# Optimization experiments

Hardware: AMD Instinct MI355X
Metric: run time of the kernel (lower is better)

The kernel has to match this reference:

```python
import jax, jax.numpy as jnp
import numpy as np
from jax import lax

B, C, IMG, P = 32, 3, 224, 16
W, L, H, E = 768, 12, 12, 512
S = (IMG // P) ** 2 + 1  # 197
HD = W // H  # 64
FF = 4 * W


def _make_pe():
    pos = np.arange(S, dtype=np.float64)[:, None]
    i = np.arange(W, dtype=np.float64)[None, :]
    angle = pos / 10000.0 ** ((i - (i % 2)) / W)
    pe = np.where(i % 2 == 0, np.sin(angle), np.cos(angle))
    return jnp.asarray(pe[None], dtype=jnp.float32)  # [1,S,W]


def setup_inputs() -> dict:
    key = jax.random.key(0)
    ks = iter(jax.random.split(key, 32))
    g = lambda shape, s=0.02: jax.random.normal(next(ks), shape, jnp.float32) * s
    return {
        "x": jax.random.normal(next(ks), (B, C, IMG, IMG), jnp.float32),
        "conv_w": g((W, C, P, P)),
        "conv_b": jnp.zeros((W,), jnp.float32),
        "cls_token": g((1, 1, W), 1.0),
        "pe": _make_pe(),
        "ln1_g": jnp.ones((L, W), jnp.float32),
        "ln1_b": jnp.zeros((L, W), jnp.float32),
        "wq": g((L, W, W)), "bq": jnp.zeros((L, W), jnp.float32),
        "wk": g((L, W, W)), "bk": jnp.zeros((L, W), jnp.float32),
        "wv": g((L, W, W)), "bv": jnp.zeros((L, W), jnp.float32),
        "wo": g((L, W, W)), "bo": jnp.zeros((L, W), jnp.float32),
        "ln2_g": jnp.ones((L, W), jnp.float32),
        "ln2_b": jnp.zeros((L, W), jnp.float32),
        "w1": g((L, W, FF)), "b1": jnp.zeros((L, FF), jnp.float32),
        "w2": g((L, FF, W)), "b2": jnp.zeros((L, W), jnp.float32),
        "proj": g((W, E), 1.0),
    }


def _layernorm(x, gamma, beta, eps=1e-5):
    m = jnp.mean(x, axis=-1, keepdims=True)
    v = jnp.mean((x - m) ** 2, axis=-1, keepdims=True)
    return (x - m) * lax.rsqrt(v + eps) * gamma + beta


def _forward(x, conv_w, conv_b, cls_token, pe, ln1_g, ln1_b, wq, bq, wk, bk,
             wv, bv, wo, bo, ln2_g, ln2_b, w1, b1, w2, b2, proj):
    # patch embedding: conv stride = patch size
    p = lax.conv_general_dilated(x, conv_w, (P, P), 'VALID',
                                 dimension_numbers=('NCHW', 'OIHW', 'NCHW'))
    p = p + conv_b[None, :, None, None]
    tokens = p.reshape(p.shape[0], W, -1).transpose(0, 2, 1)  # [B, n_patches, W]
    cls = jnp.broadcast_to(cls_token, (tokens.shape[0], 1, W))
    h = jnp.concatenate([cls, tokens], axis=1) + pe  # [B,S,W]

    def block(h, params):
        (g1, b1_, Wq, Bq, Wk, Bk, Wv, Bv, Wo, Bo, g2, b2_, W1, B1, W2, B2) = params
        y = _layernorm(h, g1, b1_)
        q = (y @ Wq + Bq).reshape(-1, S, H, HD)
        k = (y @ Wk + Bk).reshape(-1, S, H, HD)
        v = (y @ Wv + Bv).reshape(-1, S, H, HD)
        att = jnp.einsum('bshd,bthd->bhst', q, k) / jnp.sqrt(jnp.float32(HD))
        att = jax.nn.softmax(att, axis=-1)
        o = jnp.einsum('bhst,bthd->bshd', att, v).reshape(-1, S, W)
        h = h + o @ Wo + Bo
        y = _layernorm(h, g2, b2_)
        h = h + jax.nn.gelu(y @ W1 + B1, approximate=False) @ W2 + B2
        return h, None

    stacked = (ln1_g, ln1_b, wq, bq, wk, bk, wv, bv, wo, bo,
               ln2_g, ln2_b, w1, b1, w2, b2)
    h, _ = lax.scan(block, h, stacked)
    out = h[:, 0] @ proj  # [B,E]
    return out / jnp.linalg.norm(out, axis=-1, keepdims=True)


def reference(x, conv_w, conv_b, cls_token, pe, ln1_g, ln1_b, wq, bq, wk, bk,
              wv, bv, wo, bo, ln2_g, ln2_b, w1, b1, w2, b2, proj):
    return _forward(x, conv_w, conv_b, cls_token, pe, ln1_g, ln1_b, wq, bq,
                    wk, bk, wv, bv, wo, bo, ln2_g, ln2_b, w1, b1, w2, b2, proj)
```

## Files before the change

### kernel.cpp

```cpp
#include <hip/hip_runtime.h>
#include <math.h>

#define NB 32
#define SEQ 197
#define WD 768
#define NH 12
#define HD 64
#define FF 3072
#define NL 12
#define ROWS (NB*SEQ)
#define MPAD 6400
#define PROWS (NB*196)

typedef __attribute__((ext_vector_type(8))) short short8x;
typedef __attribute__((ext_vector_type(4))) float f32x4;

__device__ __forceinline__ ushort f2bf(float f) {
  unsigned u = __builtin_bit_cast(unsigned, f);
  u += 0x7fffu + ((u >> 16) & 1u);
  return (ushort)(u >> 16);
}

__device__ __forceinline__ void gload16(const ushort* g, ushort* l) {
  __builtin_amdgcn_global_load_lds(
      (const __attribute__((address_space(1))) void*)g,
      (__attribute__((address_space(3))) void*)l, 16, 0, 0);
}

__device__ __forceinline__ float wave_sum(float v) {
  #pragma unroll
  for (int off = 32; off; off >>= 1) v += __shfl_xor(v, off);
  return v;
}

template<int EPI>
__global__ __launch_bounds__(256) void gemm_bt(
    const ushort* __restrict__ A, const ushort* __restrict__ Bt,
    const float* __restrict__ bias, const float* __restrict__ R,
    float* __restrict__ Cf, ushort* __restrict__ Cb,
    int M, int N, int K)
{
  __shared__ __align__(16) ushort As[128*32];
  __shared__ __align__(16) ushort Bs[128*32];
  const int tid = threadIdx.x;
  const int gx = gridDim.x;
  const int nwg = gx * gridDim.y;
  const int orig = blockIdx.y * gx + blockIdx.x;
  const int xcd = orig & 7, lin = orig >> 3;
  const int qq = nwg >> 3, rr = nwg & 7;
  const int id = xcd*qq + (xcd < rr ? xcd : rr) + lin;
  const int bm = (id / gx) * 128;
  const int bn = (id % gx) * 128;

  const int w = tid >> 6, ln = tid & 63;
  const int wr = (w >> 1) * 64, wc = (w & 1) * 64;
  const int srow = tid >> 2, skoff = (tid & 3) * 8;
  const ushort* Ap = A + (size_t)(bm + srow) * K + skoff;
  const ushort* Bp = Bt + (size_t)(bn + srow) * K + skoff;
  ushort* AsW = As + w * 512;
  ushort* BsW = Bs + w * 512;
  const size_t half = (size_t)64 * K;
  const int fr = ln & 15, kg = ln >> 4;

  f32x4 acc[4][4];
  #pragma unroll
  for (int m = 0; m < 4; ++m)
    #pragma unroll
    for (int n = 0; n < 4; ++n) acc[m][n] = (f32x4){0.f, 0.f, 0.f, 0.f};

  for (int k0 = 0; k0 < K; k0 += 32) {
    __syncthreads();
    gload16(Ap + k0, AsW);
    gload16(Ap + half + k0, AsW + 2048);
    gload16(Bp + k0, BsW);
    gload16(Bp + half + k0, BsW + 2048);
    __syncthreads();
    short8x av[4], bv[4];
    #pragma unroll
    for (int m = 0; m < 4; ++m)
      av[m] = *(const short8x*)&As[(wr + m*16 + fr)*32 + kg*8];
    #pragma unroll
    for (int n = 0; n < 4; ++n)
      bv[n] = *(const short8x*)&Bs[(wc + n*16 + fr)*32 + kg*8];
    #pragma unroll
    for (int m = 0; m < 4; ++m)
      #pragma unroll
      for (int n = 0; n < 4; ++n)
        acc[m][n] = __builtin_amdgcn_mfma_f32_16x16x32_bf16(av[m], bv[n], acc[m][n], 0, 0, 0);
  }

  const int crow = bm + wr + kg*4;
  const int ccol = bn + wc + fr;
  float bi[4];
  #pragma unroll
  for (int n = 0; n < 4; ++n) bi[n] = bias[ccol + n*16];
  #pragma unroll
  for (int m = 0; m < 4; ++m) {
    #pragma unroll
    for (int j = 0; j < 4; ++j) {
      const int r = crow + m*16 + j;
      if (r < M) {
        #pragma unroll
        for (int n = 0; n < 4; ++n) {
          const size_t off = (size_t)r * N + ccol + n*16;
          float vv = acc[m][n][j] + bi[n];
          if (EPI == 0) Cf[off] = vv;
          if (EPI == 1) Cf[off] = vv + R[off];
          if (EPI == 2) Cb[off] = f2bf(0.5f * vv * (1.f + erff(vv * 0.70710678118654752f)));
          if (EPI == 3) Cb[off] = f2bf(vv);
        }
      }
    }
  }
}

__global__ __launch_bounds__(256) void attn_fused(
    const ushort* __restrict__ qkv,
    ushort* __restrict__ obf)
{
  __shared__ __align__(16) ushort KP[208*72];
  __shared__ __align__(16) ushort Vt[64*232];
  const int tid = threadIdx.x;
  const int w = tid >> 6, l = tid & 63;
  const int fr = l & 15, kg = l >> 4;
  const int orig = blockIdx.y * 4 + blockIdx.x;
  const int id = (orig & 7) * 192 + (orig >> 3);
  const int qt = id & 3;
  const int bh = id >> 2;
  const int b = bh / 12, hh = bh - b*12;
  const size_t qrow0 = (size_t)b * SEQ;
  const ushort* kbase = qkv + qrow0*2304 + 768 + hh*64;
  const ushort* vbase = qkv + qrow0*2304 + 1536 + hh*64;

  #pragma unroll
  for (int it = 0; it < 7; ++it) {
    const int idx = it*256 + tid;
    if (idx < 1664) {
      const int row = idx >> 3, kc = (idx & 7) << 3;
      short8x v = (short8x){0,0,0,0,0,0,0,0};
      if (row < SEQ) v = *(const short8x*)(kbase + (size_t)row*2304 + kc);
      *(short8x*)&KP[row*72 + kc] = v;
    }
  }
  #pragma unroll
  for (int it = 0; it < 7; ++it) {
    const int t = it*32 + (tid & 31);
    const int dc = ((tid >> 5) & 7) << 3;
    short8x v = (short8x){0,0,0,0,0,0,0,0};
    if (t < SEQ) v = *(const short8x*)(vbase + (size_t)t*2304 + dc);
    #pragma unroll
    for (int j = 0; j < 8; ++j) Vt[(dc + j)*232 + t] = (ushort)v[j];
  }
  const int s_l = qt*64 + w*16 + fr;
  const ushort* qbase = qkv + (qrow0 + (s_l < SEQ ? s_l : SEQ-1))*2304 + hh*64;
  const short8x qf0 = *(const short8x*)(qbase + kg*8);
  const short8x qf1 = *(const short8x*)(qbase + 32 + kg*8);
  __syncthreads();

  f32x4 sacc[13];
  #pragma unroll
  for (int f = 0; f < 13; ++f) sacc[f] = (f32x4){0.f,0.f,0.f,0.f};
  #pragma unroll
  for (int f = 0; f < 13; ++f) {
    const short8x kf0 = *(const short8x*)&KP[(f*16 + fr)*72 + kg*8];
    const short8x kf1 = *(const short8x*)&KP[(f*16 + fr)*72 + 32 + kg*8];
    sacc[f] = __builtin_amdgcn_mfma_f32_16x16x32_bf16(qf0, kf0, sacc[f], 0, 0, 0);
    sacc[f] = __builtin_amdgcn_mfma_f32_16x16x32_bf16(qf1, kf1, sacc[f], 0, 0, 0);
  }
  float mx[4] = {-1e30f,-1e30f,-1e30f,-1e30f};
  #pragma unroll
  for (int f = 0; f < 13; ++f)
    #pragma unroll
    for (int j = 0; j < 4; ++j) {
      float v = sacc[f][j] * 0.125f;
      if (f == 12 && fr >= 5) v = -1e30f;
      sacc[f][j] = v;
      mx[j] = fmaxf(mx[j], v);
    }
  #pragma unroll
  for (int j = 0; j < 4; ++j) {
    mx[j] = fmaxf(mx[j], __shfl_xor(mx[j], 1));
    mx[j] = fmaxf(mx[j], __shfl_xor(mx[j], 2));
    mx[j] = fmaxf(mx[j], __shfl_xor(mx[j], 4));
    mx[j] = fmaxf(mx[j], __shfl_xor(mx[j], 8));
  }
  float sm[4] = {0.f,0.f,0.f,0.f};
  #pragma unroll
  for (int f = 0; f < 13; ++f)
    #pragma unroll
    for (int j = 0; j < 4; ++j) {
      const float e = __expf(sacc[f][j] - mx[j]);
      sacc[f][j] = e; sm[j] += e;
    }
  #pragma unroll
  for (int j = 0; j < 4; ++j) {
    sm[j] += __shfl_xor(sm[j], 1);
    sm[j] += __shfl_xor(sm[j], 2);
    sm[j] += __shfl_xor(sm[j], 4);
    sm[j] += __shfl_xor(sm[j], 8);
    sm[j] = 1.f / sm[j];
  }
  __syncthreads();
  ushort* P = &KP[w*16*232];
  #pragma unroll
  for (int f = 0; f < 13; ++f)
    #pragma unroll
    for (int j = 0; j < 4; ++j)
      P[(kg*4 + j)*232 + f*16 + fr] = f2bf(sacc[f][j] * sm[j]);
  #pragma unroll
  for (int j = 0; j < 4; ++j)
    P[(kg*4 + j)*232 + 208 + fr] = 0;
  __syncthreads();

  short8x pf[7];
  #pragma unroll
  for (int tc = 0; tc < 7; ++tc)
    pf[tc] = *(const short8x*)&P[fr*232 + tc*32 + kg*8];
  f32x4 oacc[4];
  #pragma unroll
  for (int df = 0; df < 4; ++df) oacc[df] = (f32x4){0.f,0.f,0.f,0.f};
  #pragma unroll
  for (int df = 0; df < 4; ++df)
    #pragma unroll
    for (int tc = 0; tc < 7; ++tc) {
      const short8x vf = *(const short8x*)&Vt[(df*16 + fr)*232 + tc*32 + kg*8];
      oacc[df] = __builtin_amdgcn_mfma_f32_16x16x32_bf16(pf[tc], vf, oacc[df], 0, 0, 0);
    }
  #pragma unroll
  for (int df = 0; df < 4; ++df)
    #pragma unroll
    for (int j = 0; j < 4; ++j) {
      const int s = qt*64 + w*16 + kg*4 + j;
      if (s < SEQ)
        obf[(qrow0 + s)*768 + hh*64 + df*16 + fr] = f2bf(oacc[df][j]);
    }
}

__global__ void tcast_k(const float* __restrict__ in, ushort* __restrict__ out,
                        int K, int N) {
  __shared__ float t[32][33];
  const int bx = blockIdx.x * 32, by = blockIdx.y * 32;
  const int tx = threadIdx.x, ty = threadIdx.y;
  #pragma unroll
  for (int j = 0; j < 32; j += 8)
    t[ty + j][tx] = in[(size_t)(by + ty + j) * N + bx + tx];
  __syncthreads();
  #pragma unroll
  for (int j = 0; j < 32; j += 8)
    out[(size_t)(bx + ty + j) * K + by + tx] = f2bf(t[tx][ty + j]);
}

__global__ void tcast4_k(const float* __restrict__ s0, const float* __restrict__ s1,
                         const float* __restrict__ s2, const float* __restrict__ s3,
                         ushort* __restrict__ d0, ushort* __restrict__ d1,
                         ushort* __restrict__ d2, ushort* __restrict__ d3) {
  const int z = blockIdx.z;
  const float* s = (z == 0) ? s0 : (z == 1) ? s1 : (z == 2) ? s2 : s3;
  ushort* d = (z == 0) ? d0 : (z == 1) ? d1 : (z == 2) ? d2 : d3;
  __shared__ float t[32][33];
  const int bx = blockIdx.x * 32, by = blockIdx.y * 32;
  const int tx = threadIdx.x, ty = threadIdx.y;
  #pragma unroll
  for (int j = 0; j < 32; j += 8)
    t[ty + j][tx] = s[(size_t)(by + ty + j) * WD + bx + tx];
  __syncthreads();
  #pragma unroll
  for (int j = 0; j < 32; j += 8)
    d[(size_t)(bx + ty + j) * WD + by + tx] = f2bf(t[tx][ty + j]);
}

__global__ void castcv_k(const float* __restrict__ in, ushort* __restrict__ out) {
  const int i = blockIdx.x * 256 + threadIdx.x;
  out[i] = f2bf(in[i]);
}

__global__ void bcat_k(const float* __restrict__ a, const float* __restrict__ b,
                       const float* __restrict__ c, float* __restrict__ d) {
  const int i = blockIdx.x * 256 + threadIdx.x;
  if (i < 2304) d[i] = (i < 768) ? a[i] : (i < 1536) ? b[i - 768] : c[i - 1536];
}

__global__ void im2col_k(const float* __restrict__ x, ushort* __restrict__ A) {
  const int idx = blockIdx.x * 256 + threadIdx.x;
  if (idx >= PROWS * WD) return;
  const int k = idx % WD;
  const int row = idx / WD;
  const int pw = k & 15, ph = (k >> 4) & 15, c = k >> 8;
  const int px = row % 14, py = (row / 14) % 14, b = row / 196;
  A[idx] = f2bf(x[(size_t)((b*3 + c)*224 + py*16 + ph) * 224 + px*16 + pw]);
}

__global__ void assemble_k(const float* __restrict__ tok, const float* __restrict__ cls,
                           const float* __restrict__ pe, float* __restrict__ h) {
  const int idx = blockIdx.x * 256 + threadIdx.x;
  if (idx >= ROWS * WD) return;
  const int w = idx % WD;
  const int bs = idx / WD;
  const int s = bs % SEQ;
  const int b = bs / SEQ;
  float v;
  if (s == 0) v = cls[w];
  else        v = tok[(size_t)(b*196 + s - 1) * WD + w];
  h[idx] = v + pe[(size_t)s * WD + w];
}

__global__ __launch_bounds__(256) void layernorm_k(
    const float* __restrict__ x, const float* __restrict__ g,
    const float* __restrict__ bb, ushort* __restrict__ y)
{
  const int row = blockIdx.x;
  const int tid = threadIdx.x;
  const float* xr = x + (size_t)row * WD;
  const float v0 = xr[tid], v1 = xr[tid+256], v2 = xr[tid+512];
  __shared__ float red[4];
  float s = v0 + v1 + v2;
  s = wave_sum(s);
  const int wv = tid >> 6, ln = tid & 63;
  if (ln == 0) red[wv] = s;
  __syncthreads();
  const float mean = (red[0]+red[1]+red[2]+red[3]) * (1.f/768.f);
  const float d0 = v0-mean, d1 = v1-mean, d2 = v2-mean;
  float sq = d0*d0 + d1*d1 + d2*d2;
  sq = wave_sum(sq);
  __syncthreads();
  if (ln == 0) red[wv] = sq;
  __syncthreads();
  const float var = (red[0]+red[1]+red[2]+red[3]) * (1.f/768.f);
  const float inv = rsqrtf(var + 1e-5f);
  ushort* yr = y + (size_t)row * WD;
  yr[tid]     = f2bf(d0 * inv * g[tid]     + bb[tid]);
  yr[tid+256] = f2bf(d1 * inv * g[tid+256] + bb[tid+256]);
  yr[tid+512] = f2bf(d2 * inv * g[tid+512] + bb[tid+512]);
}

__global__ __launch_bounds__(256) void head_k(
    const float* __restrict__ h, const float* __restrict__ proj,
    float* __restrict__ out)
{
  const int b = blockIdx.x;
  const int tid = threadIdx.x;
  __shared__ float hr[768];
  __shared__ float red[4];
  const float* hrow = h + (size_t)b * SEQ * WD;
  hr[tid] = hrow[tid]; hr[tid+256] = hrow[tid+256]; hr[tid+512] = hrow[tid+512];
  __syncthreads();
  float o0 = 0.f, o1 = 0.f;
  for (int kx = 0; kx < 768; ++kx) {
    const float hv = hr[kx];
    o0 = fmaf(hv, proj[(size_t)kx*512 + tid],       o0);
    o1 = fmaf(hv, proj[(size_t)kx*512 + tid + 256], o1);
  }
  float sq = o0*o0 + o1*o1;
  sq = wave_sum(sq);
  const int wv = tid >> 6, ln = tid & 63;
  if (ln == 0) red[wv] = sq;
  __syncthreads();
  const float inv = 1.f / sqrtf(red[0]+red[1]+red[2]+red[3]);
  out[(size_t)b*512 + tid]       = o0 * inv;
  out[(size_t)b*512 + tid + 256] = o1 * inv;
}

extern "C" void kernel_launch(void* const* d_in, const int* in_sizes, int n_in,
                              void* d_out, int out_size, void* d_ws, size_t ws_size,
                              hipStream_t stream) {
  const float* x      = (const float*)d_in[0];
  const float* conv_w = (const float*)d_in[1];
  const float* conv_b = (const float*)d_in[2];
  const float* cls    = (const float*)d_in[3];
  const float* pe     = (const float*)d_in[4];
  const float* ln1_g  = (const float*)d_in[5];
  const float* ln1_b  = (const float*)d_in[6];
  const float* wq = (const float*)d_in[7];  const float* bq = (const float*)d_in[8];
  const float* wk = (const float*)d_in[9];  const float* bk = (const float*)d_in[10];
  const float* wvw = (const float*)d_in[11]; const float* bv = (const float*)d_in[12];
  const float* wo = (const float*)d_in[13]; const float* bo = (const float*)d_in[14];
  const float* ln2_g = (const float*)d_in[15]; const float* ln2_b = (const float*)d_in[16];
  const float* w1 = (const float*)d_in[17]; const float* b1 = (const float*)d_in[18];
  const float* w2 = (const float*)d_in[19]; const float* b2 = (const float*)d_in[20];
  const float* proj = (const float*)d_in[21];
  float* out = (float*)d_out;

  float* ws = (float*)d_ws;
  const size_t TOK = (size_t)ROWS * WD;
  float* h = ws;
  ushort* ub = (ushort*)(ws + TOK);
  ushort* ybf    = ub;  ub += (size_t)MPAD * WD;
  ushort* qkv    = ub;  ub += (size_t)MPAD * 2304;
  ushort* obf    = ub;  ub += (size_t)MPAD * WD;
  ushort* zbf    = ub;  ub += (size_t)MPAD * FF;
  ushort* wt_qkv = ub;  ub += (size_t)2304 * WD;
  ushort* wt_o   = ub;  ub += (size_t)WD * WD;
  ushort* wt_1   = ub;  ub += (size_t)WD * FF;
  ushort* wt_2   = ub;  ub += (size_t)FF * WD;
  float* bqkv = (float*)ub;  ub += 4608;
  ushort* imbf   = zbf;
  float*  ypatch = (float*)(zbf + (size_t)PROWS * WD);
  ushort* cbf    = wt_qkv;

  castcv_k<<<dim3(2304), dim3(256), 0, stream>>>(conv_w, cbf);
  im2col_k<<<dim3((PROWS*WD)/256), dim3(256), 0, stream>>>(x, imbf);
  gemm_bt<0><<<dim3(6, 49), dim3(256), 0, stream>>>(
      imbf, cbf, conv_b, nullptr, ypatch, nullptr, PROWS, WD, WD);
  assemble_k<<<dim3((ROWS*WD)/256), dim3(256), 0, stream>>>(ypatch, cls, pe, h);

  const dim3 gqkv(18, 50);
  const dim3 g768(6, 50);
  const dim3 gff(24, 50);
  const dim3 gattn(4, NB*NH);
  const dim3 tdim(32, 8);

  for (int l = 0; l < NL; ++l) {
    const size_t wOff = (size_t)l * WD * WD;
    const size_t fOff = (size_t)l * WD * FF;
    const size_t vOff = (size_t)l * WD;
    const size_t fvOff = (size_t)l * FF;

    tcast4_k<<<dim3(24,24,4), tdim, 0, stream>>>(
        wq+wOff, wk+wOff, wvw+wOff, wo+wOff,
        wt_qkv, wt_qkv + 589824, wt_qkv + 1179648, wt_o);
    tcast_k<<<dim3(96,24), tdim, 0, stream>>>(w1+fOff, wt_1, WD, FF);
    tcast_k<<<dim3(24,96), tdim, 0, stream>>>(w2+fOff, wt_2, FF, WD);
    bcat_k<<<dim3(9), dim3(256), 0, stream>>>(bq+vOff, bk+vOff, bv+vOff, bqkv);

    layernorm_k<<<dim3(ROWS), dim3(256), 0, stream>>>(h, ln1_g+vOff, ln1_b+vOff, ybf);
    gemm_bt<3><<<gqkv, dim3(256), 0, stream>>>(ybf, wt_qkv, bqkv, nullptr,
                                               nullptr, qkv, ROWS, 2304, WD);
    attn_fused<<<gattn, dim3(256), 0, stream>>>(qkv, obf);
    gemm_bt<1><<<g768, dim3(256), 0, stream>>>(obf, wt_o, bo+vOff, h, h, nullptr, ROWS, WD, WD);
    layernorm_k<<<dim3(ROWS), dim3(256), 0, stream>>>(h, ln2_g+vOff, ln2_b+vOff, ybf);
    gemm_bt<2><<<gff, dim3(256), 0, stream>>>(ybf, wt_1, b1+fvOff, nullptr,
                                              nullptr, zbf, ROWS, FF, WD);
    gemm_bt<1><<<g768, dim3(256), 0, stream>>>(zbf, wt_2, b2+vOff, h, h, nullptr, ROWS, WD, FF);
  }

  head_k<<<dim3(NB), dim3(256), 0, stream>>>(h, proj, out);
}
```

Before: 3.540 ms.

## Double-buffer GEMM LDS tiles and split-K the N=768 projections with combine kernel

The GEMM mainloop now double-buffers its LDS tiles, issuing the next K-slice's global-to-LDS loads before computing the current one, so there is one barrier per iteration instead of two. The two N=768 GEMMs (attention output projection and FFN down-projection) are split over K into two halves via blockIdx.z. This doubles their grid from 300 workgroups, which is meant to fill the MI355X CUs better. The halves write fp32 partial planes, and a new combine kernel adds both partials, the bias and the residual into h. The split adds extra global traffic for the partials and extra launches, and doubles LDS use per block, which may lower occupancy.

```diff
diff --git a/kernel.cpp b/kernel.cpp
--- a/kernel.cpp
+++ b/kernel.cpp
@@ -38,10 +38,10 @@
     const ushort* __restrict__ A, const ushort* __restrict__ Bt,
     const float* __restrict__ bias, const float* __restrict__ R,
     float* __restrict__ Cf, ushort* __restrict__ Cb,
-    int M, int N, int K)
+    int M, int N, int K, int kspl)
 {
-  __shared__ __align__(16) ushort As[128*32];
-  __shared__ __align__(16) ushort Bs[128*32];
+  __shared__ __align__(16) ushort As[2][128*32];
+  __shared__ __align__(16) ushort Bs[2][128*32];
   const int tid = threadIdx.x;
   const int gx = gridDim.x;
   const int nwg = gx * gridDim.y;
@@ -51,14 +51,14 @@
   const int id = xcd*qq + (xcd < rr ? xcd : rr) + lin;
   const int bm = (id / gx) * 128;
   const int bn = (id % gx) * 128;
+  const int koff = blockIdx.z * kspl;
 
   const int w = tid >> 6, ln = tid & 63;
   const int wr = (w >> 1) * 64, wc = (w & 1) * 64;
   const int srow = tid >> 2, skoff = (tid & 3) * 8;
-  const ushort* Ap = A + (size_t)(bm + srow) * K + skoff;
-  const ushort* Bp = Bt + (size_t)(bn + srow) * K + skoff;
-  ushort* AsW = As + w * 512;
-  ushort* BsW = Bs + w * 512;
+  const ushort* Ap = A + (size_t)(bm + srow) * K + skoff + koff;
+  const ushort* Bp = Bt + (size_t)(bn + srow) * K + skoff + koff;
+  const int lofs = w * 512;
   const size_t half = (size_t)64 * K;
   const int fr = ln & 15, kg = ln >> 4;
 
@@ -68,32 +68,43 @@
     #pragma unroll
     for (int n = 0; n < 4; ++n) acc[m][n] = (f32x4){0.f, 0.f, 0.f, 0.f};
 
-  for (int k0 = 0; k0 < K; k0 += 32) {
-    __syncthreads();
-    gload16(Ap + k0, AsW);
-    gload16(Ap + half + k0, AsW + 2048);
-    gload16(Bp + k0, BsW);
-    gload16(Bp + half + k0, BsW + 2048);
-    __syncthreads();
+  gload16(Ap,        &As[0][lofs]);
+  gload16(Ap + half, &As[0][lofs + 2048]);
+  gload16(Bp,        &Bs[0][lofs]);
+  gload16(Bp + half, &Bs[0][lofs + 2048]);
+  __syncthreads();
+
+  const int nt = kspl >> 5;
+  for (int t = 0; t < nt; ++t) {
+    const int cur = t & 1;
+    if (t + 1 < nt) {
+      const int k1 = (t + 1) << 5;
+      gload16(Ap + k1,        &As[cur ^ 1][lofs]);
+      gload16(Ap + half + k1, &As[cur ^ 1][lofs + 2048]);
+      gload16(Bp + k1,        &Bs[cur ^ 1][lofs]);
+      gload16(Bp + half + k1, &Bs[cur ^ 1][lofs + 2048]);
+    }
     short8x av[4], bv[4];
     #pragma unroll
     for (int m = 0; m < 4; ++m)
-      av[m] = *(const short8x*)&As[(wr + m*16 + fr)*32 + kg*8];
+      av[m] = *(const short8x*)&As[cur][(wr + m*16 + fr)*32 + kg*8];
     #pragma unroll
     for (int n = 0; n < 4; ++n)
-      bv[n] = *(const short8x*)&Bs[(wc + n*16 + fr)*32 + kg*8];
+      bv[n] = *(const short8x*)&Bs[cur][(wc + n*16 + fr)*32 + kg*8];
     #pragma unroll
     for (int m = 0; m < 4; ++m)
       #pragma unroll
       for (int n = 0; n < 4; ++n)
         acc[m][n] = __builtin_amdgcn_mfma_f32_16x16x32_bf16(av[m], bv[n], acc[m][n], 0, 0, 0);
-  }
-
+    __syncthreads();
+  }
+
+  if (EPI == 4) Cf += (size_t)blockIdx.z * ((size_t)MPAD * N);
   const int crow = bm + wr + kg*4;
   const int ccol = bn + wc + fr;
   float bi[4];
   #pragma unroll
-  for (int n = 0; n < 4; ++n) bi[n] = bias[ccol + n*16];
+  for (int n = 0; n < 4; ++n) bi[n] = (EPI == 4) ? 0.f : bias[ccol + n*16];
   #pragma unroll
   for (int m = 0; m < 4; ++m) {
     #pragma unroll
@@ -108,10 +119,17 @@
           if (EPI == 1) Cf[off] = vv + R[off];
           if (EPI == 2) Cb[off] = f2bf(0.5f * vv * (1.f + erff(vv * 0.70710678118654752f)));
           if (EPI == 3) Cb[off] = f2bf(vv);
+          if (EPI == 4) Cf[off] = vv;
         }
       }
     }
   }
+}
+
+__global__ void combine_k(const float* __restrict__ p0, const float* __restrict__ p1,
+                          const float* __restrict__ bias, float* __restrict__ h) {
+  const int idx = blockIdx.x * 256 + threadIdx.x;
+  h[idx] += p0[idx] + p1[idx] + bias[idx % WD];
 }
 
 __global__ __launch_bounds__(256) void attn_fused(
@@ -382,8 +400,10 @@
 
   float* ws = (float*)d_ws;
   const size_t TOK = (size_t)ROWS * WD;
+  const size_t PPLANE = (size_t)MPAD * WD;
   float* h = ws;
-  ushort* ub = (ushort*)(ws + TOK);
+  float* part = h + TOK;
+  ushort* ub = (ushort*)(part + 2*PPLANE);
   ushort* ybf    = ub;  ub += (size_t)MPAD * WD;
   ushort* qkv    = ub;  ub += (size_t)MPAD * 2304;
   ushort* obf    = ub;  ub += (size_t)MPAD * WD;
@@ -400,13 +420,14 @@
   castcv_k<<<dim3(2304), dim3(256), 0, stream>>>(conv_w, cbf);
   im2col_k<<<dim3((PROWS*WD)/256), dim3(256), 0, stream>>>(x, imbf);
   gemm_bt<0><<<dim3(6, 49), dim3(256), 0, stream>>>(
-      imbf, cbf, conv_b, nullptr, ypatch, nullptr, PROWS, WD, WD);
+      imbf, cbf, conv_b, nullptr, ypatch, nullptr, PROWS, WD, WD, WD);
   assemble_k<<<dim3((ROWS*WD)/256), dim3(256), 0, stream>>>(ypatch, cls, pe, h);
 
   const dim3 gqkv(18, 50);
-  const dim3 g768(6, 50);
   const dim3 gff(24, 50);
+  const dim3 gsplit(6, 50, 2);
   const dim3 gattn(4, NB*NH);
+  const dim3 gcomb((ROWS*WD)/256);
   const dim3 tdim(32, 8);
 
   for (int l = 0; l < NL; ++l) {
@@ -424,13 +445,17 @@
 
     layernorm_k<<<dim3(ROWS), dim3(256), 0, stream>>>(h, ln1_g+vOff, ln1_b+vOff, ybf);
     gemm_bt<3><<<gqkv, dim3(256), 0, stream>>>(ybf, wt_qkv, bqkv, nullptr,
-                                               nullptr, qkv, ROWS, 2304, WD);
+                                               nullptr, qkv, ROWS, 2304, WD, WD);
     attn_fused<<<gattn, dim3(256), 0, stream>>>(qkv, obf);
-    gemm_bt<1><<<g768, dim3(256), 0, stream>>>(obf, wt_o, bo+vOff, h, h, nullptr, ROWS, WD, WD);
+    gemm_bt<4><<<gsplit, dim3(256), 0, stream>>>(obf, wt_o, nullptr, nullptr,
+                                                 part, nullptr, ROWS, WD, WD, WD/2);
+    combine_k<<<gcomb, dim3(256), 0, stream>>>(part, part + PPLANE, bo+vOff, h);
     layernorm_k<<<dim3(ROWS), dim3(256), 0, stream>>>(h, ln2_g+vOff, ln2_b+vOff, ybf);
     gemm_bt<2><<<gff, dim3(256), 0, stream>>>(ybf, wt_1, b1+fvOff, nullptr,
-                                              nullptr, zbf, ROWS, FF, WD);
-    gemm_bt<1><<<g768, dim3(256), 0, stream>>>(zbf, wt_2, b2+vOff, h, h, nullptr, ROWS, WD, FF);
+                                              nullptr, zbf, ROWS, FF, WD, WD);
+    gemm_bt<4><<<gsplit, dim3(256), 0, stream>>>(zbf, wt_2, nullptr, nullptr,
+                                                 part, nullptr, ROWS, WD, FF, FF/2);
+    combine_k<<<gcomb, dim3(256), 0, stream>>>(part, part + PPLANE, b2+vOff, h);
   }
 
   head_k<<<dim3(NB), dim3(256), 0, stream>>>(h, proj, out);
```

After: 3.318 ms. 1.07x faster.
